# Optimization experiments

Hardware: AMD Instinct MI355X
Metric: run time of the kernel (lower is better)

The kernel has to match this reference:

```python
import jax, jax.numpy as jnp
import numpy as np


def setup_inputs() -> dict:
    key = jax.random.key(0)
    k1, k2, k3, k4, k5, k6 = jax.random.split(key, 6)
    Ne, dim_in, dim_out, B, Nr, E = 100000, 128, 128, 4, 8, 200000
    return {
        "H": jax.random.normal(k1, (Ne, dim_in), dtype=jnp.float32),
        "A": jax.random.uniform(k2, (Nr, B), dtype=jnp.float32),
        "V": jax.random.uniform(k3, (B, dim_in, dim_out), dtype=jnp.float32),
        "edge_row": jax.random.randint(k4, (Nr, E), 0, Ne, dtype=jnp.int32),
        "edge_col": jax.random.randint(k5, (Nr, E), 0, Ne, dtype=jnp.int32),
        "edge_val": jax.random.uniform(k6, (Nr, E), dtype=jnp.float32),
    }


def reference(H, A, V, edge_row, edge_col, edge_val):
    # W = einsum('rb,bio->rio', A, V): basis-decomposed relation weights
    Ne = H.shape[0]
    Nr = A.shape[0]
    W = jnp.einsum('rb,bio->rio', A, V)            # [Nr, dim_in, dim_out]
    HxW = jnp.einsum('ni,rio->rno', H, W)          # [Nr, Ne, dim_out]
    # sparse T_r @ HxW_r: gather source rows (cols of T), scale by values,
    # scatter-add into destination rows. Done for all relations at once.
    msgs = HxW[jnp.arange(Nr)[:, None], edge_col] * edge_val[..., None]  # [Nr, E, dim_out]
    out = jax.ops.segment_sum(
        msgs.reshape(-1, msgs.shape[-1]),
        edge_row.reshape(-1),
        num_segments=Ne,
    )  # sum over relations folded into one segment_sum
    return out
```

## Files before the change

kernel.cpp:

```cpp
#include <hip/hip_runtime.h>

typedef __attribute__((ext_vector_type(8))) short short8;
typedef __attribute__((ext_vector_type(4))) float floatx4;
typedef __attribute__((ext_vector_type(2))) float floatx2;

constexpr int DIM   = 128;
constexpr int NB    = 4;
constexpr int NR    = 8;
constexpr int BROWS = 512;
constexpr int BCAP  = 16384;

static __device__ __forceinline__ unsigned short f2bf(float f) {
    unsigned int u = __float_as_uint(f);
    u += 0x7FFFu + ((u >> 16) & 1u);
    return (unsigned short)(u >> 16);
}
static __device__ __forceinline__ float bf_lo(unsigned int h) {
    return __uint_as_float(h << 16);
}
static __device__ __forceinline__ float bf_hi(unsigned int h) {
    return __uint_as_float(h & 0xFFFF0000u);
}

__global__ __launch_bounds__(256) void build_vfrag(
    const float* __restrict__ V, unsigned short* __restrict__ VfragG)
{
    int idx  = blockIdx.x * 256 + threadIdx.x;
    int lane = idx & 63;
    int ks   = (idx >> 6) & 3;
    int ot   = (idx >> 8) & 7;
    int b    = idx >> 11;

    int o  = ot * 16 + (lane & 15);
    int kb = ks * 32 + (lane >> 4) * 8;

    short8 v;
#pragma unroll
    for (int j = 0; j < 8; ++j)
        v[j] = (short)f2bf(V[((size_t)b * DIM + kb + j) * DIM + o]);
    *reinterpret_cast<short8*>(VfragG + (size_t)idx * 8) = v;
}

__global__ __launch_bounds__(256) void build_wfrag(
    const float* __restrict__ A, const float* __restrict__ V,
    unsigned short* __restrict__ Wfrag)
{
    int idx  = blockIdx.x * 256 + threadIdx.x;
    int lane = idx & 63;
    int ks   = (idx >> 6) & 3;
    int ot   = (idx >> 8) & 7;
    int r    = idx >> 11;

    int o     = ot * 16 + (lane & 15);
    int kbase = ks * 32 + (lane >> 4) * 8;

    float a0 = A[r * NB + 0], a1 = A[r * NB + 1];
    float a2 = A[r * NB + 2], a3 = A[r * NB + 3];

    short8 v;
#pragma unroll
    for (int j = 0; j < 8; ++j) {
        int k = kbase + j;
        float w = a0 * V[(0 * DIM + k) * DIM + o]
                + a1 * V[(1 * DIM + k) * DIM + o]
                + a2 * V[(2 * DIM + k) * DIM + o]
                + a3 * V[(3 * DIM + k) * DIM + o];
        v[j] = (short)f2bf(w);
    }
    *reinterpret_cast<short8*>(Wfrag + (size_t)idx * 8) = v;
}

__global__ __launch_bounds__(256) void h_to_bf(
    const float* __restrict__ H, unsigned short* __restrict__ Hbf, int n8)
{
    int i = blockIdx.x * 256 + threadIdx.x;
    if (i >= n8) return;
    const float4* hp = reinterpret_cast<const float4*>(H) + (size_t)i * 2;
    float4 f0 = hp[0];
    float4 f1 = hp[1];
    short8 v;
    v[0] = (short)f2bf(f0.x); v[1] = (short)f2bf(f0.y);
    v[2] = (short)f2bf(f0.z); v[3] = (short)f2bf(f0.w);
    v[4] = (short)f2bf(f1.x); v[5] = (short)f2bf(f1.y);
    v[6] = (short)f2bf(f1.z); v[7] = (short)f2bf(f1.w);
    *reinterpret_cast<short8*>(Hbf + (size_t)i * 8) = v;
}

__global__ __launch_bounds__(256) void bucket_scatter(
    const int* __restrict__ erow, const int* __restrict__ ecol,
    const float* __restrict__ eval, int* __restrict__ bcnt,
    int2* __restrict__ sorted1, int n, int E, int chunk)
{
    __shared__ int cnt[256];
    __shared__ int base[256];
    int t = threadIdx.x;
    cnt[t] = 0;
    __syncthreads();

    int s = blockIdx.x * chunk;
    int e = s + chunk; if (e > n) e = n;

    for (int i = s + t; i < e; i += 256)
        atomicAdd(&cnt[erow[i] >> 9], 1);
    __syncthreads();

    int c = cnt[t];
    base[t] = (c > 0) ? atomicAdd(&bcnt[t], c) : 0;
    cnt[t] = 0;
    __syncthreads();

    for (int i = s + t; i < e; i += 256) {
        int row = erow[i];
        int bkt = row >> 9;
        int rank = atomicAdd(&cnt[bkt], 1);
        int r = (int)((unsigned)i / (unsigned)E);
        int2 m;
        m.x = ((row & (BROWS - 1)) << 20) | (r << 17) | ecol[i];
        m.y = __float_as_int(eval[i]);
        sorted1[(size_t)bkt * BCAP + base[bkt] + rank] = m;
    }
}

__global__ __launch_bounds__(1024) void bucket_sort(
    const int2* __restrict__ sorted1, const int* __restrict__ bcnt,
    int* __restrict__ rowStart, int2* __restrict__ sorted, int Ne, int nbuc)
{
    __shared__ int hcnt[BROWS];
    __shared__ int hoff[BROWS];
    __shared__ int sd[256];
    int b = blockIdx.x;
    int t = threadIdx.x;

    for (int i = t; i < BROWS; i += 1024) hcnt[i] = 0;

    if (t < 256) sd[t] = (t < nbuc) ? bcnt[t] : 0;
    __syncthreads();
#pragma unroll
    for (int off = 1; off < 256; off <<= 1) {
        int v = (t < 256 && t >= off) ? sd[t - off] : 0;
        __syncthreads();
        if (t < 256) sd[t] += v;
        __syncthreads();
    }
    if (b == 0 && t == nbuc - 1) rowStart[Ne] = sd[t];

    int n  = bcnt[b];
    int bs = sd[b] - n;
    const int2* src = sorted1 + (size_t)b * BCAP;

    for (int i = t; i < n; i += 1024)
        atomicAdd(&hcnt[(unsigned)src[i].x >> 20], 1);
    __syncthreads();

    if (t < BROWS) hoff[t] = hcnt[t];
    __syncthreads();
#pragma unroll
    for (int off = 1; off < BROWS; off <<= 1) {
        int v = (t < BROWS && t >= off) ? hoff[t - off] : 0;
        __syncthreads();
        if (t < BROWS) hoff[t] += v;
        __syncthreads();
    }
    if (t < BROWS) hoff[t] -= hcnt[t];
    __syncthreads();

    int rs = b * BROWS;
    int nr = Ne - rs; if (nr > BROWS) nr = BROWS;
    for (int j = t; j < nr; j += 1024)
        rowStart[rs + j] = bs + hoff[j];

    for (int i = t; i < BROWS; i += 1024) hcnt[i] = 0;
    __syncthreads();

    for (int i = t; i < n; i += 1024) {
        int2 m = src[i];
        int lr = (unsigned)m.x >> 20;
        int pos = bs + hoff[lr] + atomicAdd(&hcnt[lr], 1);
        sorted[pos] = m;
    }
}

#define AGG_LOAD8(kk, vv, hh, base)                                          \
    _Pragma("unroll")                                                        \
    for (int u = 0; u < 8; ++u) {                                            \
        int2 m = sorted[(base) + u];                                         \
        kk[u] = __builtin_amdgcn_readfirstlane(m.x);                         \
        vv[u] = __uint_as_float(__builtin_amdgcn_readfirstlane(m.y));        \
    }                                                                        \
    _Pragma("unroll")                                                        \
    for (int u = 0; u < 8; ++u)                                              \
        hh[u] = reinterpret_cast<const unsigned int*>(                       \
            Hbf + (size_t)(kk[u] & 0x1FFFF) * DIM)[lane];

#define AGG_FMA8(kk, vv, hh)                                                 \
    _Pragma("unroll")                                                        \
    for (int u = 0; u < 8; ++u) {                                            \
        float4 a = Af[((unsigned)kk[u] >> 17) & 7];                          \
        floatx2 h; h[0] = bf_lo(hh[u]); h[1] = bf_hi(hh[u]);                 \
        float s0 = vv[u] * a.x, s1 = vv[u] * a.y;                            \
        float s2 = vv[u] * a.z, s3 = vv[u] * a.w;                            \
        acc[0] += (floatx2){s0, s0} * h;                                     \
        acc[1] += (floatx2){s1, s1} * h;                                     \
        acc[2] += (floatx2){s2, s2} * h;                                     \
        acc[3] += (floatx2){s3, s3} * h;                                     \
    }

__global__ __launch_bounds__(256) void agg_kernel(
    const unsigned short* __restrict__ Hbf,
    const int*  __restrict__ rowStart,
    const int2* __restrict__ sorted,
    const float* __restrict__ Aw,
    unsigned short* __restrict__ AggT, int Ne)
{
    int tid  = threadIdx.x;
    int wid  = __builtin_amdgcn_readfirstlane(blockIdx.x * 4 + (tid >> 6));
    if (wid >= Ne) return;
    int lane = tid & 63;

    int s = __builtin_amdgcn_readfirstlane(rowStart[wid]);
    int e = __builtin_amdgcn_readfirstlane(rowStart[wid + 1]);

    const float4* Af = reinterpret_cast<const float4*>(Aw);

    floatx2 acc[4];
#pragma unroll
    for (int b = 0; b < 4; ++b) acc[b] = (floatx2){0.f, 0.f};

    int i = s;
    if (i + 8 <= e) {
        int kkA[8], kkB[8];
        float vvA[8], vvB[8];
        unsigned int hhA[8], hhB[8];
        AGG_LOAD8(kkA, vvA, hhA, i); i += 8;
        for (;;) {
            if (i + 8 <= e) {
                AGG_LOAD8(kkB, vvB, hhB, i); i += 8;
                AGG_FMA8(kkA, vvA, hhA);
            } else { AGG_FMA8(kkA, vvA, hhA); break; }
            if (i + 8 <= e) {
                AGG_LOAD8(kkA, vvA, hhA, i); i += 8;
                AGG_FMA8(kkB, vvB, hhB);
            } else { AGG_FMA8(kkB, vvB, hhB); break; }
        }
    }
    for (; i < e; ++i) {
        int2 m = sorted[i];
        int k = __builtin_amdgcn_readfirstlane(m.x);
        float v = __uint_as_float(__builtin_amdgcn_readfirstlane(m.y));
        unsigned int hu = reinterpret_cast<const unsigned int*>(
            Hbf + (size_t)(k & 0x1FFFF) * DIM)[lane];
        float4 a = Af[((unsigned)k >> 17) & 7];
        floatx2 h; h[0] = bf_lo(hu); h[1] = bf_hi(hu);
        float s0 = v * a.x, s1 = v * a.y, s2 = v * a.z, s3 = v * a.w;
        acc[0] += (floatx2){s0, s0} * h;
        acc[1] += (floatx2){s1, s1} * h;
        acc[2] += (floatx2){s2, s2} * h;
        acc[3] += (floatx2){s3, s3} * h;
    }

    int t = wid >> 4, r = wid & 15;
    size_t base = (size_t)t * 8192 + (size_t)r * 32
                + (size_t)(lane >> 4) * 512
                + (size_t)((lane >> 2) & 3) * 8
                + (size_t)(lane & 3) * 2;
    unsigned short* arow = AggT + base;
#pragma unroll
    for (int b = 0; b < 4; ++b) {
        unsigned int pk = (unsigned int)f2bf(acc[b][0])
                        | ((unsigned int)f2bf(acc[b][1]) << 16);
        *reinterpret_cast<unsigned int*>(arow + b * 2048) = pk;
    }
}

__global__ __launch_bounds__(512) void vgemm_kernel(
    const unsigned short* __restrict__ AggT,
    const unsigned short* __restrict__ VfragG,
    float* __restrict__ out, int Ne, int nTiles)
{
    __shared__ short8 ldsV[4096];
    int half = (blockIdx.x >> 3) & 1;
    int blk  = ((blockIdx.x >> 4) << 3) | (blockIdx.x & 7);
    int nblk = gridDim.x >> 1;
    int tid  = threadIdx.x;

    for (int i = tid; i < 4096; i += 512) {
        int lane = i & 63, ks = (i >> 6) & 3, otl = (i >> 8) & 3, b = i >> 10;
        int gi = ((b * 8 + half * 4 + otl) * 4 + ks) * 64 + lane;
        ldsV[i] = reinterpret_cast<const short8*>(VfragG)[gi];
    }
    __syncthreads();

    int wave = tid >> 6;
    int lane = tid & 63;
    int quad = lane >> 4, l15 = lane & 15;

    int wgid = blk * 8 + wave;
    int nw   = nblk * 8;

    const short8* AggV = reinterpret_cast<const short8*>(AggT);

    for (int tile = wgid; tile < nTiles; tile += nw) {
        int node = tile * 16 + l15;

        const short8* bp = AggV + (size_t)tile * 1024 + l15 * 4 + quad;
        short8 bf[16];
#pragma unroll
        for (int b = 0; b < 4; ++b)
#pragma unroll
            for (int ks = 0; ks < 4; ++ks)
                bf[b * 4 + ks] = bp[b * 256 + ks * 64];

        floatx4 acc[4];
#pragma unroll
        for (int o = 0; o < 4; ++o) acc[o] = (floatx4){0.f, 0.f, 0.f, 0.f};

#pragma unroll
        for (int b = 0; b < 4; ++b)
#pragma unroll
            for (int ks = 0; ks < 4; ++ks)
#pragma unroll
                for (int otl = 0; otl < 4; ++otl)
                    acc[otl] = __builtin_amdgcn_mfma_f32_16x16x32_bf16(
                        ldsV[((b * 4 + otl) * 4 + ks) * 64 + lane],
                        bf[b * 4 + ks], acc[otl], 0, 0, 0);

        if (node < Ne) {
            float* orow = out + (size_t)node * DIM + half * 64;
#pragma unroll
            for (int otl = 0; otl < 4; ++otl) {
                float4 st;
                st.x = acc[otl][0]; st.y = acc[otl][1];
                st.z = acc[otl][2]; st.w = acc[otl][3];
                *reinterpret_cast<float4*>(orow + otl * 16 + quad * 4) = st;
            }
        }
    }
}

__global__ __launch_bounds__(256) void rgcn_main(
    const unsigned short* __restrict__ Hbf,
    const unsigned short* __restrict__ Wfrag,
    const int*   __restrict__ erow,
    const int*   __restrict__ ecol,
    const float* __restrict__ eval,
    float*       __restrict__ out,
    int E, int groups_per_rel, int waves_per_rel)
{
    int wid  = blockIdx.x * 4 + (threadIdx.x >> 6);
    int lane = threadIdx.x & 63;
    int r    = wid & 7;
    int wr   = wid >> 3;
    int quad = lane >> 4;
    int l15  = lane & 15;

    short8 b[8][4];
    {
        const short8* wp = reinterpret_cast<const short8*>(
            Wfrag + (size_t)r * 16384);
#pragma unroll
        for (int ot = 0; ot < 8; ++ot)
#pragma unroll
            for (int ks = 0; ks < 4; ++ks)
                b[ot][ks] = wp[(ot * 4 + ks) * 64 + lane];
    }

    for (int g = wr; g < groups_per_rel; g += waves_per_rel) {
        int ebase = r * E + g * 16;
        int   colv = ecol[ebase + l15];
        int   rowv = erow[ebase + l15];
        float valv = eval[ebase + l15];

        short8 a[4];
        const unsigned short* hp = Hbf + (size_t)colv * DIM + quad * 8;
#pragma unroll
        for (int ks = 0; ks < 4; ++ks)
            a[ks] = *reinterpret_cast<const short8*>(hp + ks * 32);

        floatx4 acc[8];
#pragma unroll
        for (int ot = 0; ot < 8; ++ot) acc[ot] = (floatx4){0.f, 0.f, 0.f, 0.f};
#pragma unroll
        for (int ot = 0; ot < 8; ++ot)
#pragma unroll
            for (int ks = 0; ks < 4; ++ks)
                acc[ot] = __builtin_amdgcn_mfma_f32_16x16x32_bf16(
                    a[ks], b[ot][ks], acc[ot], 0, 0, 0);

        int   row4[4];
        float val4[4];
#pragma unroll
        for (int reg = 0; reg < 4; ++reg) {
            int src  = quad * 4 + reg;
            row4[reg] = __shfl(rowv, src, 64);
            val4[reg] = __shfl(valv, src, 64);
        }
#pragma unroll
        for (int ot = 0; ot < 8; ++ot)
#pragma unroll
            for (int reg = 0; reg < 4; ++reg) {
                float m = acc[ot][reg] * val4[reg];
                atomicAdd(out + (size_t)row4[reg] * DIM + ot * 16 + l15, m);
            }
    }
}

extern "C" void kernel_launch(void* const* d_in, const int* in_sizes, int n_in,
                              void* d_out, int out_size, void* d_ws, size_t ws_size,
                              hipStream_t stream)
{
    const float* H    = (const float*)d_in[0];
    const float* A    = (const float*)d_in[1];
    const float* V    = (const float*)d_in[2];
    const int*   erow = (const int*)d_in[3];
    const int*   ecol = (const int*)d_in[4];
    const float* eval = (const float*)d_in[5];
    float* out = (float*)d_out;

    int Ne    = in_sizes[0] / DIM;
    int NEtot = in_sizes[3];
    int E     = NEtot / NR;

    auto al = [](size_t x) { return (x + 255) & ~(size_t)255; };

    int nbuc = (Ne + BROWS - 1) / BROWS;
    int nTiles = (Ne + 15) / 16;

    size_t offHbf    = 0;
    size_t offVfrag  = offHbf    + al((size_t)Ne * DIM * 2);
    size_t offWfrag  = offVfrag  + al((size_t)8192 * 16);
    size_t offAgg    = offWfrag  + al((size_t)16384 * 16);
    size_t offRow    = offAgg    + al((size_t)nTiles * 16384);
    size_t offBcnt   = offRow    + al(((size_t)Ne + 2) * 4);
    size_t offSort   = offBcnt   + al((size_t)256 * 4);
    size_t total     = offSort   + al((size_t)NEtot * 8);

    char* ws = (char*)d_ws;
    unsigned short* Hbf    = (unsigned short*)(ws + offHbf);
    unsigned short* VfragG = (unsigned short*)(ws + offVfrag);
    unsigned short* Wfrag  = (unsigned short*)(ws + offWfrag);

    int n8 = Ne * DIM / 8;
    h_to_bf<<<(n8 + 255) / 256, 256, 0, stream>>>(H, Hbf, n8);

    if (ws_size < total) {
        build_wfrag<<<64, 256, 0, stream>>>(A, V, Wfrag);
        hipMemsetAsync(d_out, 0, (size_t)Ne * DIM * sizeof(float), stream);
        int blocks = 4096;
        int waves_per_rel = blocks * 4 / NR;
        int groups_per_rel = E / 16;
        rgcn_main<<<blocks, 256, 0, stream>>>(Hbf, Wfrag, erow, ecol, eval, out,
                                              E, groups_per_rel, waves_per_rel);
        return;
    }

    unsigned short* AggT     = (unsigned short*)(ws + offAgg);
    int2*           sorted1  = (int2*)(ws + offAgg);
    int*            rowStart = (int*)(ws + offRow);
    int*            bcnt     = (int*)(ws + offBcnt);
    int2*           sorted   = (int2*)(ws + offSort);

    build_vfrag<<<32, 256, 0, stream>>>(V, VfragG);

    hipMemsetAsync(bcnt, 0, 256 * 4, stream);
    int sblocks = 1024;
    int chunk   = (NEtot + sblocks - 1) / sblocks;
    bucket_scatter<<<sblocks, 256, 0, stream>>>(erow, ecol, eval, bcnt,
                                                sorted1, NEtot, E, chunk);
    bucket_sort<<<nbuc, 1024, 0, stream>>>(sorted1, bcnt, rowStart,
                                           sorted, Ne, nbuc);

    agg_kernel<<<(Ne + 3) / 4, 256, 0, stream>>>(Hbf, rowStart, sorted, A,
                                                 AggT, Ne);

    vgemm_kernel<<<512, 512, 0, stream>>>(AggT, VfragG, out, Ne, nTiles);
}
```

Measured before the change: 322.4 us.

## Fuse neighbor aggregation and basis GEMM into one persistent LDS-staged kernel

```diff
diff --git a/kernel.cpp b/kernel.cpp
--- a/kernel.cpp
+++ b/kernel.cpp
@@ -205,135 +205,103 @@
         acc[3] += (floatx2){s3, s3} * h;                                     \
     }
 
-__global__ __launch_bounds__(256) void agg_kernel(
+__global__ __launch_bounds__(1024, 4) void fused_kernel(
     const unsigned short* __restrict__ Hbf,
     const int*  __restrict__ rowStart,
     const int2* __restrict__ sorted,
     const float* __restrict__ Aw,
-    unsigned short* __restrict__ AggT, int Ne)
-{
-    int tid  = threadIdx.x;
-    int wid  = __builtin_amdgcn_readfirstlane(blockIdx.x * 4 + (tid >> 6));
-    if (wid >= Ne) return;
-    int lane = tid & 63;
-
-    int s = __builtin_amdgcn_readfirstlane(rowStart[wid]);
-    int e = __builtin_amdgcn_readfirstlane(rowStart[wid + 1]);
-
-    const float4* Af = reinterpret_cast<const float4*>(Aw);
-
-    floatx2 acc[4];
-#pragma unroll
-    for (int b = 0; b < 4; ++b) acc[b] = (floatx2){0.f, 0.f};
-
-    int i = s;
-    if (i + 8 <= e) {
-        int kkA[8], kkB[8];
-        float vvA[8], vvB[8];
-        unsigned int hhA[8], hhB[8];
-        AGG_LOAD8(kkA, vvA, hhA, i); i += 8;
-        for (;;) {
-            if (i + 8 <= e) {
-                AGG_LOAD8(kkB, vvB, hhB, i); i += 8;
-                AGG_FMA8(kkA, vvA, hhA);
-            } else { AGG_FMA8(kkA, vvA, hhA); break; }
-            if (i + 8 <= e) {
-                AGG_LOAD8(kkA, vvA, hhA, i); i += 8;
-                AGG_FMA8(kkB, vvB, hhB);
-            } else { AGG_FMA8(kkB, vvB, hhB); break; }
-        }
-    }
-    for (; i < e; ++i) {
-        int2 m = sorted[i];
-        int k = __builtin_amdgcn_readfirstlane(m.x);
-        float v = __uint_as_float(__builtin_amdgcn_readfirstlane(m.y));
-        unsigned int hu = reinterpret_cast<const unsigned int*>(
-            Hbf + (size_t)(k & 0x1FFFF) * DIM)[lane];
-        float4 a = Af[((unsigned)k >> 17) & 7];
-        floatx2 h; h[0] = bf_lo(hu); h[1] = bf_hi(hu);
-        float s0 = v * a.x, s1 = v * a.y, s2 = v * a.z, s3 = v * a.w;
-        acc[0] += (floatx2){s0, s0} * h;
-        acc[1] += (floatx2){s1, s1} * h;
-        acc[2] += (floatx2){s2, s2} * h;
-        acc[3] += (floatx2){s3, s3} * h;
-    }
-
-    int t = wid >> 4, r = wid & 15;
-    size_t base = (size_t)t * 8192 + (size_t)r * 32
-                + (size_t)(lane >> 4) * 512
-                + (size_t)((lane >> 2) & 3) * 8
-                + (size_t)(lane & 3) * 2;
-    unsigned short* arow = AggT + base;
-#pragma unroll
-    for (int b = 0; b < 4; ++b) {
-        unsigned int pk = (unsigned int)f2bf(acc[b][0])
-                        | ((unsigned int)f2bf(acc[b][1]) << 16);
-        *reinterpret_cast<unsigned int*>(arow + b * 2048) = pk;
-    }
-}
-
-__global__ __launch_bounds__(512) void vgemm_kernel(
-    const unsigned short* __restrict__ AggT,
     const unsigned short* __restrict__ VfragG,
     float* __restrict__ out, int Ne, int nTiles)
 {
-    __shared__ short8 ldsV[4096];
-    int half = (blockIdx.x >> 3) & 1;
-    int blk  = ((blockIdx.x >> 4) << 3) | (blockIdx.x & 7);
-    int nblk = gridDim.x >> 1;
+    __shared__ short8 ldsV[8192];
+    __shared__ unsigned short ldsA[8192];
+
     int tid  = threadIdx.x;
-
-    for (int i = tid; i < 4096; i += 512) {
-        int lane = i & 63, ks = (i >> 6) & 3, otl = (i >> 8) & 3, b = i >> 10;
-        int gi = ((b * 8 + half * 4 + otl) * 4 + ks) * 64 + lane;
-        ldsV[i] = reinterpret_cast<const short8*>(VfragG)[gi];
-    }
-    __syncthreads();
-
     int wave = tid >> 6;
     int lane = tid & 63;
     int quad = lane >> 4, l15 = lane & 15;
 
-    int wgid = blk * 8 + wave;
-    int nw   = nblk * 8;
-
-    const short8* AggV = reinterpret_cast<const short8*>(AggT);
-
-    for (int tile = wgid; tile < nTiles; tile += nw) {
-        int node = tile * 16 + l15;
-
-        const short8* bp = AggV + (size_t)tile * 1024 + l15 * 4 + quad;
-        short8 bf[16];
-#pragma unroll
-        for (int b = 0; b < 4; ++b)
-#pragma unroll
-            for (int ks = 0; ks < 4; ++ks)
-                bf[b * 4 + ks] = bp[b * 256 + ks * 64];
-
-        floatx4 acc[4];
-#pragma unroll
-        for (int o = 0; o < 4; ++o) acc[o] = (floatx4){0.f, 0.f, 0.f, 0.f};
-
-#pragma unroll
-        for (int b = 0; b < 4; ++b)
-#pragma unroll
-            for (int ks = 0; ks < 4; ++ks)
-#pragma unroll
-                for (int otl = 0; otl < 4; ++otl)
-                    acc[otl] = __builtin_amdgcn_mfma_f32_16x16x32_bf16(
-                        ldsV[((b * 4 + otl) * 4 + ks) * 64 + lane],
-                        bf[b * 4 + ks], acc[otl], 0, 0, 0);
+    for (int i = tid; i < 8192; i += 1024)
+        ldsV[i] = reinterpret_cast<const short8*>(VfragG)[i];
+
+    const float4* Af = reinterpret_cast<const float4*>(Aw);
+
+    unsigned short* aw = ldsA + (size_t)wave * 32
+                       + (size_t)(lane >> 4) * 512
+                       + (size_t)((lane >> 2) & 3) * 8
+                       + (size_t)(lane & 3) * 2;
+
+    for (int tile = blockIdx.x; tile < nTiles; tile += gridDim.x) {
+        int node = tile * 16 + wave;
+        floatx2 acc[4];
+#pragma unroll
+        for (int b = 0; b < 4; ++b) acc[b] = (floatx2){0.f, 0.f};
 
         if (node < Ne) {
-            float* orow = out + (size_t)node * DIM + half * 64;
-#pragma unroll
-            for (int otl = 0; otl < 4; ++otl) {
-                float4 st;
-                st.x = acc[otl][0]; st.y = acc[otl][1];
-                st.z = acc[otl][2]; st.w = acc[otl][3];
-                *reinterpret_cast<float4*>(orow + otl * 16 + quad * 4) = st;
+            int s = __builtin_amdgcn_readfirstlane(rowStart[node]);
+            int e = __builtin_amdgcn_readfirstlane(rowStart[node + 1]);
+            int i = s;
+            if (i + 8 <= e) {
+                int kkA[8], kkB[8];
+                float vvA[8], vvB[8];
+                unsigned int hhA[8], hhB[8];
+                AGG_LOAD8(kkA, vvA, hhA, i); i += 8;
+                for (;;) {
+                    if (i + 8 <= e) {
+                        AGG_LOAD8(kkB, vvB, hhB, i); i += 8;
+                        AGG_FMA8(kkA, vvA, hhA);
+                    } else { AGG_FMA8(kkA, vvA, hhA); break; }
+                    if (i + 8 <= e) {
+                        AGG_LOAD8(kkA, vvA, hhA, i); i += 8;
+                        AGG_FMA8(kkB, vvB, hhB);
+                    } else { AGG_FMA8(kkB, vvB, hhB); break; }
+                }
+            }
+            for (; i < e; ++i) {
+                int2 m = sorted[i];
+                int k = __builtin_amdgcn_readfirstlane(m.x);
+                float v = __uint_as_float(__builtin_amdgcn_readfirstlane(m.y));
+                unsigned int hu = reinterpret_cast<const unsigned int*>(
+                    Hbf + (size_t)(k & 0x1FFFF) * DIM)[lane];
+                float4 a = Af[((unsigned)k >> 17) & 7];
+                floatx2 h; h[0] = bf_lo(hu); h[1] = bf_hi(hu);
+                float s0 = v * a.x, s1 = v * a.y, s2 = v * a.z, s3 = v * a.w;
+                acc[0] += (floatx2){s0, s0} * h;
+                acc[1] += (floatx2){s1, s1} * h;
+                acc[2] += (floatx2){s2, s2} * h;
+                acc[3] += (floatx2){s3, s3} * h;
             }
         }
+#pragma unroll
+        for (int b = 0; b < 4; ++b) {
+            unsigned int pk = (unsigned int)f2bf(acc[b][0])
+                            | ((unsigned int)f2bf(acc[b][1]) << 16);
+            *reinterpret_cast<unsigned int*>(aw + b * 2048) = pk;
+        }
+        __syncthreads();
+
+        if (wave < 8) {
+            int ot = wave;
+            const short8* a8 = reinterpret_cast<const short8*>(ldsA);
+            floatx4 vacc = (floatx4){0.f, 0.f, 0.f, 0.f};
+#pragma unroll
+            for (int b = 0; b < 4; ++b)
+#pragma unroll
+                for (int ks = 0; ks < 4; ++ks)
+                    vacc = __builtin_amdgcn_mfma_f32_16x16x32_bf16(
+                        ldsV[((b * 8 + ot) * 4 + ks) * 64 + lane],
+                        a8[b * 256 + ks * 64 + l15 * 4 + quad],
+                        vacc, 0, 0, 0);
+
+            int onode = tile * 16 + l15;
+            if (onode < Ne) {
+                float4 st;
+                st.x = vacc[0]; st.y = vacc[1]; st.z = vacc[2]; st.w = vacc[3];
+                *reinterpret_cast<float4*>(
+                    out + (size_t)onode * DIM + ot * 16 + quad * 4) = st;
+            }
+        }
+        __syncthreads();
     }
 }
 
@@ -428,8 +396,8 @@
     size_t offHbf    = 0;
     size_t offVfrag  = offHbf    + al((size_t)Ne * DIM * 2);
     size_t offWfrag  = offVfrag  + al((size_t)8192 * 16);
-    size_t offAgg    = offWfrag  + al((size_t)16384 * 16);
-    size_t offRow    = offAgg    + al((size_t)nTiles * 16384);
+    size_t offSort1  = offWfrag  + al((size_t)16384 * 16);
+    size_t offRow    = offSort1  + al((size_t)nbuc * BCAP * 8);
     size_t offBcnt   = offRow    + al(((size_t)Ne + 2) * 4);
     size_t offSort   = offBcnt   + al((size_t)256 * 4);
     size_t total     = offSort   + al((size_t)NEtot * 8);
@@ -453,8 +421,7 @@
         return;
     }
 
-    unsigned short* AggT     = (unsigned short*)(ws + offAgg);
-    int2*           sorted1  = (int2*)(ws + offAgg);
+    int2*           sorted1  = (int2*)(ws + offSort1);
     int*            rowStart = (int*)(ws + offRow);
     int*            bcnt     = (int*)(ws + offBcnt);
     int2*           sorted   = (int2*)(ws + offSort);
@@ -469,8 +436,6 @@
     bucket_sort<<<nbuc, 1024, 0, stream>>>(sorted1, bcnt, rowStart,
                                            sorted, Ne, nbuc);
 
-    agg_kernel<<<(Ne + 3) / 4, 256, 0, stream>>>(Hbf, rowStart, sorted, A,
-                                                 AggT, Ne);
-
-    vgemm_kernel<<<512, 512, 0, stream>>>(AggT, VfragG, out, Ne, nTiles);
-}
+    fused_kernel<<<256, 1024, 0, stream>>>(Hbf, rowStart, sorted, A,
+                                           VfragG, out, Ne, nTiles);
+}
```

Result: no change. 316.7 us (-1.8%).
